# Performance work log

Measured on AMD Instinct MI355X. Metric: run time of the kernel, lower is better.

## Reference

```python
import jax, jax.numpy as jnp
import numpy as np

B, DIM, H, W = 8, 96, 256, 256
NH, WS, SS = 3, 8, 4
HD = DIM // NH
SCALE = HD ** -0.5
N = WS * WS  # tokens per window


def _rel_pos_log(ws):
    # [N, N, 2] signed log relative coordinates (matches get_relative_positions)
    coords = np.stack(np.meshgrid(np.arange(ws), np.arange(ws), indexing='ij'))
    cf = coords.reshape(2, -1)
    rel = (cf[:, :, None] - cf[:, None, :]).transpose(1, 2, 0).astype(np.float32)
    return np.sign(rel) * np.log1p(np.abs(rel))


def _attn_mask(Hh, Ww, ws, ss):
    # Swin shifted-window mask: [nW, N, N] with 0 / -100
    img = np.zeros((Hh, Ww))
    cnt = 0
    sl = (slice(0, -ws), slice(-ws, -ss), slice(-ss, None))
    for h in sl:
        for w in sl:
            img[h, w] = cnt
            cnt += 1
    mw = img.reshape(Hh // ws, ws, Ww // ws, ws).transpose(0, 2, 1, 3).reshape(-1, ws * ws)
    am = mw[:, None, :] - mw[:, :, None]
    return np.where(am != 0, -100.0, 0.0).astype(np.float32)


REL_POS = jnp.asarray(_rel_pos_log(WS))        # [N, N, 2]
ATTN_MASK = jnp.asarray(_attn_mask(H, W, WS, SS))  # [nW, N, N]


def setup_inputs() -> dict:
    key = jax.random.key(0)
    ks = jax.random.split(key, 8)
    s = 0.02
    return {
        'x': jax.random.normal(ks[0], (B, DIM, H, W), jnp.float32),
        'V_w': jax.random.normal(ks[1], (DIM, DIM), jnp.float32) * s,
        'V_b': jnp.zeros((DIM,), jnp.float32),
        'QK_w': jax.random.normal(ks[2], (2 * DIM, DIM), jnp.float32) * s,
        'QK_b': jnp.zeros((2 * DIM,), jnp.float32),
        'proj_w': jax.random.normal(ks[3], (DIM, DIM), jnp.float32) * s,
        'proj_b': jnp.zeros((DIM,), jnp.float32),
        'dw_w': jax.random.normal(ks[4], (DIM, 5, 5), jnp.float32) * s,
        'dw_b': jnp.zeros((DIM,), jnp.float32),
        'meta_w1': jax.random.normal(ks[5], (256, 2), jnp.float32) * 0.1,
        'meta_b1': jnp.zeros((256,), jnp.float32),
        'meta_w2': jax.random.normal(ks[6], (NH, 256), jnp.float32) * 0.1,
        'meta_b2': jnp.zeros((NH,), jnp.float32),
    }


def reference(x, V_w, V_b, QK_w, QK_b, proj_w, proj_b, dw_w, dw_b,
              meta_w1, meta_b1, meta_w2, meta_b2):
    # 1x1 convs as channel matmuls
    V = jnp.einsum('bchw,oc->bohw', x, V_w) + V_b[None, :, None, None]
    QK = jnp.einsum('bchw,oc->bohw', x, QK_w) + QK_b[None, :, None, None]
    qkv = jnp.concatenate([QK, V], axis=1).transpose(0, 2, 3, 1)  # [B,H,W,3C]
    # cyclic shift
    qkv = jnp.roll(qkv, (-SS, -SS), axis=(1, 2))
    # window partition -> [B*nW, N, 3C]
    xw = qkv.reshape(B, H // WS, WS, W // WS, WS, 3 * DIM)
    xw = xw.transpose(0, 1, 3, 2, 4, 5).reshape(-1, N, 3 * DIM)
    qkv3 = xw.reshape(-1, N, 3, NH, HD).transpose(2, 0, 3, 1, 4)  # [3, B_, nh, N, hd]
    q, k, v = qkv3[0] * SCALE, qkv3[1], qkv3[2]
    attn = jnp.einsum('whnd,whmd->whnm', q, k)  # [B_, nh, N, N]
    # MLP relative-position bias
    bias = jax.nn.relu(REL_POS @ meta_w1.T + meta_b1) @ meta_w2.T + meta_b2  # [N,N,nh]
    attn = attn + bias.transpose(2, 0, 1)[None]
    nW = ATTN_MASK.shape[0]
    attn = attn.reshape(B, nW, NH, N, N) + ATTN_MASK[None, :, None]
    attn = jax.nn.softmax(attn, axis=-1).reshape(-1, NH, N, N)
    xo = jnp.einsum('whnm,whmd->wnhd', attn, v).reshape(-1, N, DIM)
    # window reverse -> [B,H,W,C]
    xr = xo.reshape(B, H // WS, W // WS, WS, WS, DIM)
    xr = xr.transpose(0, 1, 3, 2, 4, 5).reshape(B, H, W, DIM)
    xr = jnp.roll(xr, (SS, SS), axis=(1, 2)).transpose(0, 3, 1, 2)  # [B,C,H,W]
    # depthwise 5x5 conv with reflect padding on V
    Vp = jnp.pad(V, ((0, 0), (0, 0), (2, 2), (2, 2)), mode='reflect')
    conv_out = jax.lax.conv_general_dilated(
        Vp, dw_w.reshape(DIM, 1, 5, 5), (1, 1), 'VALID',
        feature_group_count=DIM,
        dimension_numbers=('NCHW', 'OIHW', 'NCHW')) + dw_b[None, :, None, None]
    out = jnp.einsum('bchw,oc->bohw', conv_out + xr, proj_w) + proj_b[None, :, None, None]
    return out
```

## Files before the change

kernel.cpp:

```cpp
#include <hip/hip_runtime.h>
#include <hip/hip_bf16.h>

#define HW 65536
#define SCALE_Q 0.17677669529663687f

typedef __bf16 bf16x8 __attribute__((ext_vector_type(8)));
typedef float f32x4 __attribute__((ext_vector_type(4)));

__global__ void bias_kernel(const float* __restrict__ w1, const float* __restrict__ b1,
                            const float* __restrict__ w2, const float* __restrict__ b2,
                            float* __restrict__ biasF) {
    int gid = blockIdx.x * blockDim.x + threadIdx.x;
    if (gid >= 12288) return;
    int lane = gid & 63, r = (gid >> 6) & 3, ni = (gid >> 8) & 3, mi = (gid >> 10) & 3, h = gid >> 12;
    int i = mi * 16 + ((lane >> 4) << 2) + r;
    int j = ni * 16 + (lane & 15);
    float di = (float)((i >> 3) - (j >> 3));
    float dj = (float)((i & 7) - (j & 7));
    float r0 = (di > 0.f ? 1.f : (di < 0.f ? -1.f : 0.f)) * log1pf(fabsf(di));
    float r1 = (dj > 0.f ? 1.f : (dj < 0.f ? -1.f : 0.f)) * log1pf(fabsf(dj));
    float acc = 0.f;
    for (int t = 0; t < 256; ++t) {
        float u = fmaf(w1[2 * t], r0, fmaf(w1[2 * t + 1], r1, b1[t]));
        u = fmaxf(u, 0.f);
        acc = fmaf(w2[h * 256 + t], u, acc);
    }
    biasF[gid] = acc + b2[h];
}

__global__ void wtrans_kernel(const float* __restrict__ QK_w, const float* __restrict__ V_w,
                              const float* __restrict__ proj_w,
                              __bf16* __restrict__ Whi, __bf16* __restrict__ Wlo,
                              float* __restrict__ WTproj) {
    int idx = blockIdx.x * blockDim.x + threadIdx.x;
    if (idx < 288 * 96) {
        int oo = idx / 96, c = idx - oo * 96;
        int h = oo / 96, rem = oo - h * 96, grp = rem >> 5, d = rem & 31;
        float w = (grp == 0) ? QK_w[(h * 32 + d) * 96 + c]
                : (grp == 1) ? QK_w[(96 + h * 32 + d) * 96 + c]
                             : V_w[(h * 32 + d) * 96 + c];
        __bf16 hi = (__bf16)w;
        Whi[idx] = hi;
        Wlo[idx] = (__bf16)(w - (float)hi);
    } else if (idx < 288 * 96 + 96 * 96) {
        int rdx = idx - 288 * 96;
        int c = rdx / 96, o = rdx - c * 96;
        WTproj[rdx] = proj_w[o * 96 + c];
    }
}

__global__ __launch_bounds__(256, 3) void fused_qkv_attn(
    const float* __restrict__ x,
    const __bf16* __restrict__ Whi, const __bf16* __restrict__ Wlo,
    const float* __restrict__ QK_b, const float* __restrict__ V_b,
    const float* __restrict__ biasF,
    unsigned short* __restrict__ Vout, float* __restrict__ xr) {
    __shared__ __align__(16) char lds[53376];
    int tid = threadIdx.x;
    int w4 = tid >> 6;
    int lane = tid & 63;
    int l16 = lane & 15;
    int g8 = (lane >> 4) << 3;
    int g4 = (lane >> 4) << 2;
    int bx0 = blockIdx.x;
    int bxs = (bx0 & 7) * 256 + (bx0 >> 3);
    int b = bxs >> 8;
    int wh = (bxs >> 3) & 31;
    int ww0 = (bxs & 7) << 2;
    int wh8 = wh << 3;
    int wb8 = ww0 << 3;
    int ww = ww0 + w4;
    int ti = lane >> 3, tj = lane & 7;
    int ph = (wh8 + ti + 4) & 255;
    int pw = ((ww << 3) + tj + 4) & 255;
    int pos   = ph * 256 + pw;
    int pos_s = (wh8 + ti) * 256 + (ww << 3) + tj;

    __bf16* Xh = (__bf16*)lds;
    const float* xb = x + (size_t)b * 96 * HW;
    for (int idx = tid; idx < 24576; idx += 256) {
        int c = idx >> 8, r = (idx >> 5) & 7, col = idx & 31;
        int pph = (wh8 + r + 4) & 255;
        int ppw = (wb8 + col + 4) & 255;
        Xh[(col >> 3) * 6672 + (r * 8 + (col & 7)) * 104 + c] =
            (__bf16)xb[(size_t)c * HW + pph * 256 + ppw];
    }
    __syncthreads();

    bf16x8 Ah[4][3];
    const __bf16* Xw = Xh + w4 * 6672;
#pragma unroll
    for (int mi = 0; mi < 4; ++mi)
#pragma unroll
        for (int ks = 0; ks < 3; ++ks)
            Ah[mi][ks] = *(const bf16x8*)(Xw + (mi * 16 + l16) * 104 + ks * 32 + g8);
    __syncthreads();

    char* hb = lds + w4 * 9984;
    __bf16* slab = (__bf16*)hb;
    __bf16* Vt   = (__bf16*)(hb + 5120);
    float*  Xr   = (float*)hb;

    bool bhh = (wh == 31), bww = (ww == 31);
    int rc[4];
#pragma unroll
    for (int ni = 0; ni < 4; ++ni) {
        int t = ni * 16 + l16;
        rc[ni] = (bhh ? (((t >> 3) < 4) ? 1 : 2) : 0) * 3 + (bww ? (((t & 7) < 4) ? 1 : 2) : 0);
    }

#pragma unroll 1
    for (int h = 0; h < 3; ++h) {
        bf16x8 Qf[4], Kf[4];
        {
            f32x4 acc[4][2];
#pragma unroll
            for (int mi = 0; mi < 4; ++mi)
#pragma unroll
                for (int ni = 0; ni < 2; ++ni) acc[mi][ni] = (f32x4){0.f, 0.f, 0.f, 0.f};
#pragma unroll
            for (int ks = 0; ks < 3; ++ks)
#pragma unroll
                for (int ni = 0; ni < 2; ++ni) {
                    bf16x8 Bh = *(const bf16x8*)(Whi + (h * 96 + ni * 16 + l16) * 96 + ks * 32 + g8);
#pragma unroll
                    for (int mi = 0; mi < 4; ++mi)
                        acc[mi][ni] = __builtin_amdgcn_mfma_f32_16x16x32_bf16(Ah[mi][ks], Bh, acc[mi][ni], 0, 0, 0);
                }
#pragma unroll
            for (int ni = 0; ni < 2; ++ni) {
                float bias = QK_b[h * 32 + ni * 16 + l16];
#pragma unroll
                for (int mi = 0; mi < 4; ++mi)
#pragma unroll
                    for (int r = 0; r < 4; ++r)
                        slab[(mi * 16 + g4 + r) * 40 + ni * 16 + l16] = (__bf16)((acc[mi][ni][r] + bias) * SCALE_Q);
            }
#pragma unroll
            for (int mi = 0; mi < 4; ++mi) Qf[mi] = *(const bf16x8*)(slab + (mi * 16 + l16) * 40 + g8);
        }
        {
            f32x4 acc[4][2];
#pragma unroll
            for (int mi = 0; mi < 4; ++mi)
#pragma unroll
                for (int ni = 0; ni < 2; ++ni) acc[mi][ni] = (f32x4){0.f, 0.f, 0.f, 0.f};
#pragma unroll
            for (int ks = 0; ks < 3; ++ks)
#pragma unroll
                for (int ni = 0; ni < 2; ++ni) {
                    bf16x8 Bh = *(const bf16x8*)(Whi + (h * 96 + 32 + ni * 16 + l16) * 96 + ks * 32 + g8);
#pragma unroll
                    for (int mi = 0; mi < 4; ++mi)
                        acc[mi][ni] = __builtin_amdgcn_mfma_f32_16x16x32_bf16(Ah[mi][ks], Bh, acc[mi][ni], 0, 0, 0);
                }
#pragma unroll
            for (int ni = 0; ni < 2; ++ni) {
                float bias = QK_b[96 + h * 32 + ni * 16 + l16];
#pragma unroll
                for (int mi = 0; mi < 4; ++mi)
#pragma unroll
                    for (int r = 0; r < 4; ++r)
                        slab[(mi * 16 + g4 + r) * 40 + ni * 16 + l16] = (__bf16)(acc[mi][ni][r] + bias);
            }
#pragma unroll
            for (int mi = 0; mi < 4; ++mi) Kf[mi] = *(const bf16x8*)(slab + (mi * 16 + l16) * 40 + g8);
        }
        {
            f32x4 acc[4][2];
#pragma unroll
            for (int mi = 0; mi < 4; ++mi)
#pragma unroll
                for (int ni = 0; ni < 2; ++ni) acc[mi][ni] = (f32x4){0.f, 0.f, 0.f, 0.f};
#pragma unroll
            for (int ks = 0; ks < 3; ++ks)
#pragma unroll
                for (int ni = 0; ni < 2; ++ni) {
                    int oo = (h * 96 + 64 + ni * 16 + l16) * 96 + ks * 32 + g8;
                    bf16x8 Bh = *(const bf16x8*)(Whi + oo);
                    bf16x8 Bl = *(const bf16x8*)(Wlo + oo);
#pragma unroll
                    for (int mi = 0; mi < 4; ++mi) {
                        acc[mi][ni] = __builtin_amdgcn_mfma_f32_16x16x32_bf16(Ah[mi][ks], Bh, acc[mi][ni], 0, 0, 0);
                        acc[mi][ni] = __builtin_amdgcn_mfma_f32_16x16x32_bf16(Ah[mi][ks], Bl, acc[mi][ni], 0, 0, 0);
                    }
                }
#pragma unroll
            for (int ni = 0; ni < 2; ++ni) {
                float bias = V_b[h * 32 + ni * 16 + l16];
#pragma unroll
                for (int mi = 0; mi < 4; ++mi)
#pragma unroll
                    for (int r = 0; r < 4; ++r)
                        Vt[(ni * 16 + l16) * 72 + mi * 16 + g4 + r] = (__bf16)(acc[mi][ni][r] + bias);
            }
        }
#pragma unroll
        for (int d = 0; d < 32; ++d)
            Vout[(size_t)(b * 96 + h * 32 + d) * HW + pos_s] = ((const unsigned short*)Vt)[d * 72 + lane];

        f32x4 sc[4][4];
#pragma unroll
        for (int mi = 0; mi < 4; ++mi)
#pragma unroll
            for (int ni = 0; ni < 4; ++ni) {
                sc[mi][ni] = (f32x4){0.f, 0.f, 0.f, 0.f};
                sc[mi][ni] = __builtin_amdgcn_mfma_f32_16x16x32_bf16(Qf[mi], Kf[ni], sc[mi][ni], 0, 0, 0);
            }
        const float* bF = biasF + h * 4096;
#pragma unroll
        for (int mi = 0; mi < 4; ++mi)
#pragma unroll
            for (int r = 0; r < 4; ++r) {
                int row = mi * 16 + g4 + r;
                float s0 = sc[mi][0][r] + bF[((mi * 4 + 0) * 4 + r) * 64 + lane];
                float s1 = sc[mi][1][r] + bF[((mi * 4 + 1) * 4 + r) * 64 + lane];
                float s2 = sc[mi][2][r] + bF[((mi * 4 + 2) * 4 + r) * 64 + lane];
                float s3 = sc[mi][3][r] + bF[((mi * 4 + 3) * 4 + r) * 64 + lane];
                if (bhh || bww) {
                    int rr = (bhh ? (((row >> 3) < 4) ? 1 : 2) : 0) * 3 +
                             (bww ? (((row & 7) < 4) ? 1 : 2) : 0);
                    if (rr != rc[0]) s0 -= 100.f;
                    if (rr != rc[1]) s1 -= 100.f;
                    if (rr != rc[2]) s2 -= 100.f;
                    if (rr != rc[3]) s3 -= 100.f;
                }
                float mm = fmaxf(fmaxf(s0, s1), fmaxf(s2, s3));
                mm = fmaxf(mm, __shfl_xor(mm, 1));
                mm = fmaxf(mm, __shfl_xor(mm, 2));
                mm = fmaxf(mm, __shfl_xor(mm, 4));
                mm = fmaxf(mm, __shfl_xor(mm, 8));
                float e0 = __expf(s0 - mm), e1 = __expf(s1 - mm);
                float e2 = __expf(s2 - mm), e3 = __expf(s3 - mm);
                float sum = e0 + e1 + e2 + e3;
                sum += __shfl_xor(sum, 1);
                sum += __shfl_xor(sum, 2);
                sum += __shfl_xor(sum, 4);
                sum += __shfl_xor(sum, 8);
                float inv = 1.f / sum;
                sc[mi][0][r] = e0 * inv;
                sc[mi][1][r] = e1 * inv;
                sc[mi][2][r] = e2 * inv;
                sc[mi][3][r] = e3 * inv;
            }
        f32x4 po[4][2];
#pragma unroll
        for (int mi = 0; mi < 4; ++mi)
#pragma unroll
            for (int ni = 0; ni < 2; ++ni) po[mi][ni] = (f32x4){0.f, 0.f, 0.f, 0.f};
#pragma unroll
        for (int ks = 0; ks < 2; ++ks) {
#pragma unroll
            for (int mi = 0; mi < 4; ++mi)
#pragma unroll
                for (int r = 0; r < 4; ++r) {
                    int row = mi * 16 + g4 + r;
                    slab[row * 40 + l16]      = (__bf16)sc[mi][ks * 2 + 0][r];
                    slab[row * 40 + 16 + l16] = (__bf16)sc[mi][ks * 2 + 1][r];
                }
            bf16x8 Vf[2], Pf;
#pragma unroll
            for (int ni = 0; ni < 2; ++ni)
                Vf[ni] = *(const bf16x8*)(Vt + (ni * 16 + l16) * 72 + ks * 32 + g8);
#pragma unroll
            for (int mi = 0; mi < 4; ++mi) {
                Pf = *(const bf16x8*)(slab + (mi * 16 + l16) * 40 + g8);
#pragma unroll
                for (int ni = 0; ni < 2; ++ni)
                    po[mi][ni] = __builtin_amdgcn_mfma_f32_16x16x32_bf16(Pf, Vf[ni], po[mi][ni], 0, 0, 0);
            }
        }
#pragma unroll
        for (int mi = 0; mi < 4; ++mi)
#pragma unroll
            for (int ni = 0; ni < 2; ++ni)
#pragma unroll
                for (int r = 0; r < 4; ++r)
                    Xr[(mi * 16 + g4 + r) * 36 + ni * 16 + l16] = po[mi][ni][r];
        float* xrg = xr + (size_t)(b * 96 + h * 32) * HW + pos;
#pragma unroll
        for (int c4 = 0; c4 < 8; ++c4) {
            f32x4 v = *(const f32x4*)(Xr + lane * 36 + c4 * 4);
            xrg[(size_t)(c4 * 4 + 0) * HW] = v[0];
            xrg[(size_t)(c4 * 4 + 1) * HW] = v[1];
            xrg[(size_t)(c4 * 4 + 2) * HW] = v[2];
            xrg[(size_t)(c4 * 4 + 3) * HW] = v[3];
        }
    }
}

__global__ __launch_bounds__(256) void dwproj_kernel(
    const __hip_bfloat16* __restrict__ Vs, const float* __restrict__ dw_w,
    const float* __restrict__ dw_b, const float* __restrict__ WTp,
    const float* __restrict__ pb, float* __restrict__ T) {
    __shared__ float Ts[96 * 132];
    int bx0 = blockIdx.x;
    int bx = (bx0 & 7) * 512 + (bx0 >> 3);
    int half = bx & 1, h = (bx >> 1) & 255, b = bx >> 9;
    int w0 = half << 7;
    int tid = threadIdx.x;
    for (int task = tid; task < 1536; task += 256) {
        int c = task >> 4, g = task & 15;
        int wbase = w0 + (g << 3);
        const __hip_bfloat16* Vp = Vs + (size_t)(b * 96 + c) * HW;
        const float* wt = dw_w + c * 25;
        float acc[8];
        float bias = dw_b[c];
#pragma unroll
        for (int i = 0; i < 8; ++i) acc[i] = bias;
        bool fast = (wbase >= 8) && (wbase <= 240);
#pragma unroll
        for (int dy = -2; dy <= 2; ++dy) {
            int hh = h + dy;
            hh = hh < 0 ? -hh : (hh > 255 ? 510 - hh : hh);
            int hs = (hh + 252) & 255;
            const __hip_bfloat16* row = Vp + hs * 256;
            float xv[12];
            if (fast) {
                const uint* rp = (const uint*)(row + (wbase - 6));
#pragma unroll
                for (int g2 = 0; g2 < 6; ++g2) {
                    uint u = rp[g2];
                    xv[2 * g2]     = __uint_as_float(u << 16);
                    xv[2 * g2 + 1] = __uint_as_float(u & 0xffff0000u);
                }
            } else {
#pragma unroll
                for (int idx = 0; idx < 12; ++idx) {
                    int cw = wbase - 2 + idx;
                    cw = cw < 0 ? -cw : (cw > 255 ? 510 - cw : cw);
                    int cs = (cw + 252) & 255;
                    uint u = *(const unsigned short*)(row + cs);
                    xv[idx] = __uint_as_float(u << 16);
                }
            }
            const float* w5 = wt + (dy + 2) * 5;
#pragma unroll
            for (int dx = 0; dx < 5; ++dx) {
                float wv = w5[dx];
#pragma unroll
                for (int i = 0; i < 8; ++i) acc[i] = fmaf(wv, xv[i + dx], acc[i]);
            }
        }
        const float* xp = T + (size_t)(b * 96 + c) * HW + h * 256;
        f32x4 x0 = *(const f32x4*)(xp + wbase);
        f32x4 x1 = *(const f32x4*)(xp + wbase + 4);
#pragma unroll
        for (int i = 0; i < 4; ++i) { acc[i] += x0[i]; acc[4 + i] += x1[i]; }
        float* tr = Ts + c * 132 + (g << 3);
#pragma unroll
        for (int i = 0; i < 8; ++i) tr[i] = acc[i];
    }
    __syncthreads();
    int m = tid & 127;
    int ohU = __builtin_amdgcn_readfirstlane(tid >> 7);
    for (int oc = 0; oc < 3; ++oc) {
        float acc[16];
#pragma unroll
        for (int u = 0; u < 16; ++u) acc[u] = 0.f;
        const float* wb = WTp + oc * 32 + ohU * 16;
#pragma unroll 4
        for (int c = 0; c < 96; ++c) {
            float xvv = Ts[c * 132 + m];
            const float* w = wb + c * 96;
#pragma unroll
            for (int u = 0; u < 16; ++u) acc[u] = fmaf(w[u], xvv, acc[u]);
        }
#pragma unroll
        for (int u = 0; u < 16; ++u) {
            int o = oc * 32 + ohU * 16 + u;
            T[(size_t)(b * 96 + o) * HW + h * 256 + w0 + m] = acc[u] + pb[o];
        }
    }
}

extern "C" void kernel_launch(void* const* d_in, const int* in_sizes, int n_in,
                              void* d_out, int out_size, void* d_ws, size_t ws_size,
                              hipStream_t stream) {
    const float* x      = (const float*)d_in[0];
    const float* V_w    = (const float*)d_in[1];
    const float* V_b    = (const float*)d_in[2];
    const float* QK_w   = (const float*)d_in[3];
    const float* QK_b   = (const float*)d_in[4];
    const float* proj_w = (const float*)d_in[5];
    const float* proj_b = (const float*)d_in[6];
    const float* dw_w   = (const float*)d_in[7];
    const float* dw_b   = (const float*)d_in[8];
    const float* mw1    = (const float*)d_in[9];
    const float* mb1    = (const float*)d_in[10];
    const float* mw2    = (const float*)d_in[11];
    const float* mb2    = (const float*)d_in[12];
    float* out = (float*)d_out;

    char* ws = (char*)d_ws;
    __hip_bfloat16* Vbuf = (__hip_bfloat16*)ws;
    float*  biasF = (float*)(ws + 100663296);
    __bf16* Whi   = (__bf16*)(ws + 100663296 + 49152);
    __bf16* Wlo   = (__bf16*)(ws + 100663296 + 49152 + 55296);
    float*  WTproj= (float*)(ws + 100663296 + 49152 + 55296 + 55296);

    bias_kernel<<<48, 256, 0, stream>>>(mw1, mb1, mw2, mb2, biasF);
    wtrans_kernel<<<144, 256, 0, stream>>>(QK_w, V_w, proj_w, Whi, Wlo, WTproj);
    fused_qkv_attn<<<2048, 256, 0, stream>>>(x, Whi, Wlo, QK_b, V_b, biasF,
                                             (unsigned short*)Vbuf, out);
    dwproj_kernel<<<4096, 256, 0, stream>>>(Vbuf, dw_w, dw_b, WTproj, proj_b, out);
}
```

Measured before the change: 786.5 us.

## Run output projection in dwproj on MFMA with split-bf16 precision

The 96x96 output projection in the depthwise-conv kernel moves from scalar FP32 FMAs to bf16 MFMA 16x16x32 instructions. Activations and weights are each split into hi/lo bf16 parts, and three MFMAs per tile keep near-FP32 accuracy. The LDS tile is transposed to a position-major layout with padding, weights are pre-split in the transform kernel, and outputs are written as float4 vectors. The aim is to cut the ALU-bound FMA loop, at the cost of conversion work, 3x MFMA count and a slight accuracy change.

```diff
diff --git a/kernel.cpp b/kernel.cpp
--- a/kernel.cpp
+++ b/kernel.cpp
@@ -31,7 +31,7 @@
 __global__ void wtrans_kernel(const float* __restrict__ QK_w, const float* __restrict__ V_w,
                               const float* __restrict__ proj_w,
                               __bf16* __restrict__ Whi, __bf16* __restrict__ Wlo,
-                              float* __restrict__ WTproj) {
+                              __bf16* __restrict__ WpHi, __bf16* __restrict__ WpLo) {
     int idx = blockIdx.x * blockDim.x + threadIdx.x;
     if (idx < 288 * 96) {
         int oo = idx / 96, c = idx - oo * 96;
@@ -44,8 +44,10 @@
         Wlo[idx] = (__bf16)(w - (float)hi);
     } else if (idx < 288 * 96 + 96 * 96) {
         int rdx = idx - 288 * 96;
-        int c = rdx / 96, o = rdx - c * 96;
-        WTproj[rdx] = proj_w[o * 96 + c];
+        float w = proj_w[rdx];
+        __bf16 hi = (__bf16)w;
+        WpHi[rdx] = hi;
+        WpLo[rdx] = (__bf16)(w - (float)hi);
     }
 }
 
@@ -291,9 +293,10 @@
 
 __global__ __launch_bounds__(256) void dwproj_kernel(
     const __hip_bfloat16* __restrict__ Vs, const float* __restrict__ dw_w,
-    const float* __restrict__ dw_b, const float* __restrict__ WTp,
-    const float* __restrict__ pb, float* __restrict__ T) {
-    __shared__ float Ts[96 * 132];
+    const float* __restrict__ dw_b, const __bf16* __restrict__ WpHi,
+    const __bf16* __restrict__ WpLo, const float* __restrict__ pb,
+    float* __restrict__ T) {
+    __shared__ __align__(16) float Ts[12800];
     int bx0 = blockIdx.x;
     int bx = (bx0 & 7) * 512 + (bx0 >> 3);
     int half = bx & 1, h = (bx >> 1) & 255, b = bx >> 9;
@@ -347,29 +350,62 @@
         f32x4 x1 = *(const f32x4*)(xp + wbase + 4);
 #pragma unroll
         for (int i = 0; i < 4; ++i) { acc[i] += x0[i]; acc[4 + i] += x1[i]; }
-        float* tr = Ts + c * 132 + (g << 3);
-#pragma unroll
-        for (int i = 0; i < 8; ++i) tr[i] = acc[i];
+#pragma unroll
+        for (int i = 0; i < 8; ++i) Ts[(g * 8 + i) * 100 + c] = acc[i];
     }
     __syncthreads();
-    int m = tid & 127;
-    int ohU = __builtin_amdgcn_readfirstlane(tid >> 7);
-    for (int oc = 0; oc < 3; ++oc) {
-        float acc[16];
-#pragma unroll
-        for (int u = 0; u < 16; ++u) acc[u] = 0.f;
-        const float* wb = WTp + oc * 32 + ohU * 16;
-#pragma unroll 4
-        for (int c = 0; c < 96; ++c) {
-            float xvv = Ts[c * 132 + m];
-            const float* w = wb + c * 96;
-#pragma unroll
-            for (int u = 0; u < 16; ++u) acc[u] = fmaf(w[u], xvv, acc[u]);
-        }
-#pragma unroll
-        for (int u = 0; u < 16; ++u) {
-            int o = oc * 32 + ohU * 16 + u;
-            T[(size_t)(b * 96 + o) * HW + h * 256 + w0 + m] = acc[u] + pb[o];
+    int lane = tid & 63;
+    int l16 = lane & 15;
+    int g8 = (lane >> 4) << 3;
+    int g4 = (lane >> 4) << 2;
+    int wv = tid >> 6;
+    f32x4 po[2][6];
+#pragma unroll
+    for (int mi = 0; mi < 2; ++mi)
+#pragma unroll
+        for (int ni = 0; ni < 6; ++ni) po[mi][ni] = (f32x4){0.f, 0.f, 0.f, 0.f};
+#pragma unroll
+    for (int ks = 0; ks < 3; ++ks) {
+        bf16x8 Ah[2], Al[2];
+#pragma unroll
+        for (int mi = 0; mi < 2; ++mi) {
+            const float* ap = Ts + (wv * 32 + mi * 16 + l16) * 100 + ks * 32 + g8;
+            f32x4 a0 = *(const f32x4*)ap;
+            f32x4 a1 = *(const f32x4*)(ap + 4);
+#pragma unroll
+            for (int e = 0; e < 4; ++e) {
+                float f0 = a0[e];
+                __bf16 h0 = (__bf16)f0;
+                Ah[mi][e] = h0;
+                Al[mi][e] = (__bf16)(f0 - (float)h0);
+                float f1 = a1[e];
+                __bf16 h1 = (__bf16)f1;
+                Ah[mi][4 + e] = h1;
+                Al[mi][4 + e] = (__bf16)(f1 - (float)h1);
+            }
+        }
+#pragma unroll
+        for (int ni = 0; ni < 6; ++ni) {
+            int o = ni * 16 + l16;
+            bf16x8 Bh = *(const bf16x8*)(WpHi + o * 96 + ks * 32 + g8);
+            bf16x8 Bl = *(const bf16x8*)(WpLo + o * 96 + ks * 32 + g8);
+#pragma unroll
+            for (int mi = 0; mi < 2; ++mi) {
+                po[mi][ni] = __builtin_amdgcn_mfma_f32_16x16x32_bf16(Ah[mi], Bh, po[mi][ni], 0, 0, 0);
+                po[mi][ni] = __builtin_amdgcn_mfma_f32_16x16x32_bf16(Al[mi], Bh, po[mi][ni], 0, 0, 0);
+                po[mi][ni] = __builtin_amdgcn_mfma_f32_16x16x32_bf16(Ah[mi], Bl, po[mi][ni], 0, 0, 0);
+            }
+        }
+    }
+#pragma unroll
+    for (int ni = 0; ni < 6; ++ni) {
+        int o = ni * 16 + l16;
+        float bias = pb[o];
+#pragma unroll
+        for (int mi = 0; mi < 2; ++mi) {
+            f32x4 v = po[mi][ni];
+            v[0] += bias; v[1] += bias; v[2] += bias; v[3] += bias;
+            *(f32x4*)(T + (size_t)(b * 96 + o) * HW + h * 256 + w0 + wv * 32 + mi * 16 + g4) = v;
         }
     }
 }
@@ -397,11 +433,12 @@
     float*  biasF = (float*)(ws + 100663296);
     __bf16* Whi   = (__bf16*)(ws + 100663296 + 49152);
     __bf16* Wlo   = (__bf16*)(ws + 100663296 + 49152 + 55296);
-    float*  WTproj= (float*)(ws + 100663296 + 49152 + 55296 + 55296);
+    __bf16* WpHi  = (__bf16*)(ws + 100663296 + 49152 + 2 * 55296);
+    __bf16* WpLo  = (__bf16*)(ws + 100663296 + 49152 + 2 * 55296 + 18432);
 
     bias_kernel<<<48, 256, 0, stream>>>(mw1, mb1, mw2, mb2, biasF);
-    wtrans_kernel<<<144, 256, 0, stream>>>(QK_w, V_w, proj_w, Whi, Wlo, WTproj);
+    wtrans_kernel<<<144, 256, 0, stream>>>(QK_w, V_w, proj_w, Whi, Wlo, WpHi, WpLo);
     fused_qkv_attn<<<2048, 256, 0, stream>>>(x, Whi, Wlo, QK_b, V_b, biasF,
                                              (unsigned short*)Vbuf, out);
-    dwproj_kernel<<<4096, 256, 0, stream>>>(Vbuf, dw_w, dw_b, WTproj, proj_b, out);
+    dwproj_kernel<<<4096, 256, 0, stream>>>(Vbuf, dw_w, dw_b, WpHi, WpLo, proj_b, out);
 }
```

Measured after the change: 724.7 us. -7.9%, faster.
